# Performance work log

Measured on AMD Instinct MI355X. Metric: run time of the kernel, lower is better.

The kernel has to match this reference:

```python
import jax, jax.numpy as jnp
import numpy as np

S, N, D, K, NH = 4, 32768, 256, 512, 4
HD = D // NH  # head dim 64
F = 4 * D     # ffn hidden
EPS = 1e-6


def layer_norm(x, g, b):
    mu = x.mean(-1, keepdims=True)
    var = x.var(-1, keepdims=True)
    return (x - mu) * jax.lax.rsqrt(var + 1e-5) * g + b


def setup_inputs() -> dict:
    key = jax.random.key(0)
    ks = jax.random.split(key, 16)
    w = lambda i, shape: jax.random.normal(ks[i], shape, jnp.float32) * 0.02
    return {
        "H_nodes": jax.random.normal(ks[0], (S, N, D), jnp.float32),
        "patch_ids": jax.random.randint(ks[1], (S, N), 0, K),
        "ln1_g": jnp.ones((D,), jnp.float32), "ln1_b": jnp.zeros((D,), jnp.float32),
        "Wq": w(2, (D, D)), "bq": jnp.zeros((D,), jnp.float32),
        "Wk": w(3, (D, D)), "bk": jnp.zeros((D,), jnp.float32),
        "Wv": w(4, (D, D)), "bv": jnp.zeros((D,), jnp.float32),
        "Wo": w(5, (D, D)), "bo": jnp.zeros((D,), jnp.float32),
        "ln2_g": jnp.ones((D,), jnp.float32), "ln2_b": jnp.zeros((D,), jnp.float32),
        "ffn_W1": w(6, (D, F)), "ffn_b1": jnp.zeros((F,), jnp.float32),
        "ffn_W2": w(7, (F, D)), "ffn_b2": jnp.zeros((D,), jnp.float32),
        "mlp_W1": w(8, (2 * D, D)), "mlp_b1": jnp.zeros((D,), jnp.float32),
        "mlp_W2": w(9, (D, D)), "mlp_b2": jnp.zeros((D,), jnp.float32),
    }


def reference(H_nodes, patch_ids, ln1_g, ln1_b, Wq, bq, Wk, bk, Wv, bv, Wo, bo,
              ln2_g, ln2_b, ffn_W1, ffn_b1, ffn_W2, ffn_b2,
              mlp_W1, mlp_b1, mlp_W2, mlp_b2):
    # --- segment-mean pooling by patch id (replaces double python loop) ---
    flat_ids = (patch_ids + jnp.arange(S)[:, None] * K).reshape(-1)  # [S*N]
    sums = jax.ops.segment_sum(H_nodes.reshape(S * N, D), flat_ids,
                               num_segments=S * K).reshape(S, K, D)
    counts = jax.ops.segment_sum(jnp.ones((S * N,), H_nodes.dtype), flat_ids,
                                 num_segments=S * K).reshape(S, K, 1)
    x = sums / jnp.maximum(counts, 1.0)         # empty patches stay zero
    mask = (counts > 0).astype(H_nodes.dtype)   # [S,K,1]

    # --- linear-attention transformer block over patch summaries (eval: no dropout) ---
    y = layer_norm(x, ln1_g, ln1_b)
    phi = lambda t: jax.nn.elu(t) + 1.0
    q = phi((y @ Wq + bq).reshape(S, K, NH, HD))
    k = phi((y @ Wk + bk).reshape(S, K, NH, HD)) * mask[..., None]
    v = (y @ Wv + bv).reshape(S, K, NH, HD) * mask[..., None]
    kv = jnp.einsum('skhd,skhe->shde', k, v)
    ksum = k.sum(axis=1)                                    # [S,NH,HD]
    num = jnp.einsum('skhd,shde->skhe', q, kv)
    den = jnp.einsum('skhd,shd->skh', q, ksum)[..., None] + EPS
    x = x + (num / den).reshape(S, K, D) @ Wo + bo
    y2 = layer_norm(x, ln2_g, ln2_b)
    psu = x + jax.nn.gelu(y2 @ ffn_W1 + ffn_b1, approximate=False) @ ffn_W2 + ffn_b2

    # --- gather-broadcast + concat + node MLP + residual ---
    bc = jax.vmap(lambda p, i: p[i])(psu, patch_ids)        # [S,N,D]
    combined = jnp.concatenate([H_nodes, bc], axis=-1)      # [S,N,2D]
    upd = jax.nn.gelu(combined @ mlp_W1 + mlp_b1, approximate=False) @ mlp_W2 + mlp_b2
    return H_nodes + upd, psu
```

## Files before the change

### kernel.cpp

```cpp
#include <hip/hip_runtime.h>
#include <hip/hip_bf16.h>

#define S 4
#define N 32768
#define D 256
#define KSEG 512
#define NH 4
#define HD 64
#define FF 1024

typedef __attribute__((ext_vector_type(8))) short short8;
typedef __attribute__((ext_vector_type(4))) float f32x4;
typedef __attribute__((ext_vector_type(4))) unsigned int u32x4;
typedef __attribute__((ext_vector_type(2))) unsigned int u32x2;

__device__ __forceinline__ unsigned short f2bf(float f) {
  union { __hip_bfloat16 h; unsigned short u; } cv;
  cv.h = __float2bfloat16(f);
  return cv.u;
}

__device__ __forceinline__ float gelu_f(float x) {
  return 0.5f * x * (1.0f + erff(x * 0.70710678118654752440f));
}

__device__ __forceinline__ float wave_reduce_sum(float v) {
  #pragma unroll
  for (int o = 32; o > 0; o >>= 1) v += __shfl_xor(v, o, 64);
  return v;
}

__global__ __launch_bounds__(256) void hist_kernel(
    const int* __restrict__ pids, int* __restrict__ histc)
{
  __shared__ int h[KSEG];
  int b = blockIdx.x, t = threadIdx.x;
  int s = b >> 4, c = b & 15;
  for (int i = t; i < KSEG; i += 256) h[i] = 0;
  __syncthreads();
  const int* p = pids + s * N + c * 2048;
  for (int i = t; i < 2048; i += 256) atomicAdd(&h[p[i]], 1);
  __syncthreads();
  for (int i = t; i < KSEG; i += 256) histc[(s * 16 + c) * KSEG + i] = h[i];
}

__global__ __launch_bounds__(256) void prefix_kernel(
    int* __restrict__ histc, int* __restrict__ segstart,
    int* __restrict__ cnti, float* __restrict__ counts)
{
  __shared__ int h[16 * KSEG];
  __shared__ int sc[KSEG];
  __shared__ int sa[KSEG], sb[KSEG];
  int s = blockIdx.x, t = threadIdx.x;
  for (int i = t; i < 16 * KSEG; i += 256) h[i] = histc[s * 16 * KSEG + i];
  __syncthreads();
  #pragma unroll
  for (int u = 0; u < 2; u++) {
    int bin = t + u * 256;
    int cc = 0;
    #pragma unroll
    for (int c = 0; c < 16; c++) cc += h[c * KSEG + bin];
    sc[bin] = cc;
    sa[bin] = cc;
  }
  __syncthreads();
  int* src = sa; int* dst = sb;
  for (int off = 1; off < KSEG; off <<= 1) {
    #pragma unroll
    for (int u = 0; u < 2; u++) {
      int bin = t + u * 256;
      int v = src[bin];
      if (bin >= off) v += src[bin - off];
      dst[bin] = v;
    }
    __syncthreads();
    int* tmp = src; src = dst; dst = tmp;
  }
  #pragma unroll
  for (int u = 0; u < 2; u++) {
    int bin = t + u * 256;
    int cc = sc[bin];
    int excl = src[bin] - cc;
    segstart[s * KSEG + bin] = excl;
    cnti[s * KSEG + bin] = cc;
    counts[s * KSEG + bin] = (float)cc;
    int run = excl;
    #pragma unroll
    for (int c = 0; c < 16; c++) {
      int v = h[c * KSEG + bin];
      h[c * KSEG + bin] = run;
      run += v;
    }
  }
  __syncthreads();
  for (int i = t; i < 16 * KSEG; i += 256) histc[s * 16 * KSEG + i] = h[i];
}

__global__ __launch_bounds__(256) void scatter_kernel(
    const int* __restrict__ pids, const int* __restrict__ histc,
    int* __restrict__ order)
{
  __shared__ int offs[KSEG];
  int b = blockIdx.x, t = threadIdx.x;
  int s = b >> 4, c = b & 15;
  for (int i = t; i < KSEG; i += 256) offs[i] = histc[(s * 16 + c) * KSEG + i];
  __syncthreads();
  const int* p = pids + s * N + c * 2048;
  for (int i = t; i < 2048; i += 256) {
    int pid = p[i];
    int pos = atomicAdd(&offs[pid], 1);
    order[s * N + pos] = s * N + c * 2048 + i;
  }
}

__global__ __launch_bounds__(256) void pool_gather(
    const float* __restrict__ H, const int* __restrict__ order,
    const int* __restrict__ segstart, const int* __restrict__ cnti,
    float* __restrict__ xw)
{
  __shared__ float pbuf[4][256];
  int tid = threadIdx.x;
  int w = tid >> 6, lane = tid & 63;
  int seg = blockIdx.x * 2 + (w >> 1);
  int half = w & 1;
  int s = seg >> 9;
  int st = segstart[seg], cn = cnti[seg];
  int en = st + cn;
  const int* ord = order + (size_t)s * N;
  int c4 = lane << 2;
  f32x4 a0 = {0,0,0,0}, a1 = {0,0,0,0}, a2 = {0,0,0,0}, a3 = {0,0,0,0};
  f32x4 a4 = {0,0,0,0}, a5 = {0,0,0,0}, a6 = {0,0,0,0}, a7 = {0,0,0,0};
  int i = st + half;
  for (; i + 14 < en; i += 16) {
    int r0 = ord[i + 0], r1 = ord[i + 2], r2 = ord[i + 4], r3 = ord[i + 6];
    int r4 = ord[i + 8], r5 = ord[i + 10], r6 = ord[i + 12], r7 = ord[i + 14];
    a0 += *(const f32x4*)(H + (size_t)r0 * 256 + c4);
    a1 += *(const f32x4*)(H + (size_t)r1 * 256 + c4);
    a2 += *(const f32x4*)(H + (size_t)r2 * 256 + c4);
    a3 += *(const f32x4*)(H + (size_t)r3 * 256 + c4);
    a4 += *(const f32x4*)(H + (size_t)r4 * 256 + c4);
    a5 += *(const f32x4*)(H + (size_t)r5 * 256 + c4);
    a6 += *(const f32x4*)(H + (size_t)r6 * 256 + c4);
    a7 += *(const f32x4*)(H + (size_t)r7 * 256 + c4);
  }
  for (; i < en; i += 2) {
    int r = ord[i];
    a0 += *(const f32x4*)(H + (size_t)r * 256 + c4);
  }
  f32x4 ssum = ((a0 + a1) + (a2 + a3)) + ((a4 + a5) + (a6 + a7));
  *(f32x4*)&pbuf[w][c4] = ssum;
  __syncthreads();
  if (half == 0) {
    f32x4 tot = *(f32x4*)&pbuf[w][c4];
    tot += *(f32x4*)&pbuf[w + 1][c4];
    float inv = 1.f / fmaxf((float)cn, 1.f);
    tot = tot * inv;
    *(f32x4*)(xw + (size_t)seg * 256 + c4) = tot;
  }
}

__global__ __launch_bounds__(256) void pool_ln_kernel(
    const float* __restrict__ xw,
    const float* __restrict__ g, const float* __restrict__ b,
    float* __restrict__ yw)
{
  int row = blockIdx.x, t = threadIdx.x;
  float v = xw[row * 256 + t];
  float s1 = wave_reduce_sum(v);
  float s2 = wave_reduce_sum(v * v);
  __shared__ float a1[4], a2[4];
  int w = t >> 6;
  if ((t & 63) == 0) { a1[w] = s1; a2[w] = s2; }
  __syncthreads();
  float ts1 = a1[0] + a1[1] + a1[2] + a1[3];
  float ts2 = a2[0] + a2[1] + a2[2] + a2[3];
  float mu = ts1 * (1.f / 256.f);
  float var = ts2 * (1.f / 256.f) - mu * mu;
  yw[row * 256 + t] = (v - mu) * rsqrtf(var + 1e-5f) * g[t] + b[t];
}

__global__ __launch_bounds__(256) void ln_kernel(
    const float* __restrict__ in, float* __restrict__ outp,
    const float* __restrict__ g, const float* __restrict__ b)
{
  int row = blockIdx.x, t = threadIdx.x;
  float v = in[row * 256 + t];
  float s1 = wave_reduce_sum(v);
  float s2 = wave_reduce_sum(v * v);
  __shared__ float a1[4], a2[4];
  int w = t >> 6;
  if ((t & 63) == 0) { a1[w] = s1; a2[w] = s2; }
  __syncthreads();
  float ts1 = a1[0] + a1[1] + a1[2] + a1[3];
  float ts2 = a2[0] + a2[1] + a2[2] + a2[3];
  float mu = ts1 * (1.f / 256.f);
  float var = ts2 * (1.f / 256.f) - mu * mu;
  outp[row * 256 + t] = (v - mu) * rsqrtf(var + 1e-5f) * g[t] + b[t];
}

__global__ __launch_bounds__(256) void wprep2_kernel(
    const float* __restrict__ Wq, const float* __restrict__ Wk,
    const float* __restrict__ Wv, const float* __restrict__ Wo,
    const float* __restrict__ fW1, const float* __restrict__ fW2,
    const float* __restrict__ mW1, const float* __restrict__ mW2,
    unsigned short* __restrict__ Wpack)
{
  int fi = blockIdx.x * 256 + threadIdx.x;
  const float* src; int ld, colbase, kcbits; size_t outb; int rfi;
  if (fi < 32768) {
    int m = fi >> 13; rfi = fi & 8191;
    src = (m == 0) ? Wq : ((m == 1) ? Wk : ((m == 2) ? Wv : Wo));
    ld = 256; colbase = 0; kcbits = 3; outb = (size_t)m * 65536;
  } else if (fi < 65536) {
    rfi = fi - 32768; int cc = rfi >> 13; rfi &= 8191;
    src = fW1; ld = 1024; colbase = cc * 256; kcbits = 3;
    outb = 262144 + (size_t)cc * 65536;
  } else if (fi < 98304) {
    rfi = fi - 65536; src = fW2; ld = 256; colbase = 0; kcbits = 5; outb = 524288;
  } else if (fi < 114688) {
    rfi = fi - 98304; src = mW1; ld = 256; colbase = 0; kcbits = 4; outb = 786432;
  } else {
    rfi = fi - 114688; src = mW2; ld = 256; colbase = 0; kcbits = 3; outb = 917504;
  }
  int tile = rfi >> 6, lane = rfi & 63;
  int c = tile >> kcbits, kc = tile & ((1 << kcbits) - 1);
  int k0 = kc * 32 + (lane >> 4) * 8;
  int col = colbase + c * 16 + (lane & 15);
  unsigned int p[4];
  #pragma unroll
  for (int jj = 0; jj < 4; jj++) {
    unsigned int lo = f2bf(src[(size_t)(k0 + 2 * jj) * ld + col]);
    unsigned int hi = f2bf(src[(size_t)(k0 + 2 * jj + 1) * ld + col]);
    p[jj] = lo | (hi << 16);
  }
  u32x4 v = {p[0], p[1], p[2], p[3]};
  *(u32x4*)&Wpack[outb + (size_t)rfi * 8] = v;
}

#define AP3 264
#define CP3 260

__global__ __launch_bounds__(256, 4) void qkv_mfma(
    const float* __restrict__ y, const float* __restrict__ counts,
    const unsigned short* __restrict__ Wpack,
    const float* __restrict__ bq, const float* __restrict__ bk,
    const float* __restrict__ bv,
    float* __restrict__ qo, float* __restrict__ ko, float* __restrict__ vo)
{
  __shared__ __align__(16) unsigned char smem[16 * CP3 * 4];
  unsigned short* Ah = (unsigned short*)smem;
  float* Cl = (float*)smem;
  int m = blockIdx.y;
  const unsigned short* Wf = Wpack + (size_t)m * 65536;
  const float* bias = (m == 0) ? bq : ((m == 1) ? bk : bv);
  float* outp = (m == 0) ? qo : ((m == 1) ? ko : vo);
  int tid = threadIdx.x, lane = tid & 63, w = tid >> 6;
  int ln15 = lane & 15, hi = lane >> 4;
  int base = blockIdx.x * 16;

  for (int i = tid; i < 16 * 64; i += 256) {
    int r = i >> 6, c4 = i & 63;
    float4 f = *(const float4*)(y + ((size_t)(base + r)) * 256 + c4 * 4);
    unsigned int lo = (unsigned int)f2bf(f.x) | ((unsigned int)f2bf(f.y) << 16);
    unsigned int h2 = (unsigned int)f2bf(f.z) | ((unsigned int)f2bf(f.w) << 16);
    u32x2 val = {lo, h2};
    *((u32x2*)&Ah[r * AP3 + c4 * 4]) = val;
  }
  __syncthreads();

  f32x4 acc[4];
  #pragma unroll
  for (int c = 0; c < 4; c++) acc[c] = (f32x4){0.f, 0.f, 0.f, 0.f};
  const unsigned short* Wl = Wf + (size_t)lane * 8;
  short8 bcur[4];
  #pragma unroll
  for (int ct = 0; ct < 4; ct++)
    bcur[ct] = *(const short8*)(Wl + ((w * 4 + ct) * 8 + 0) * 512);
  #pragma unroll
  for (int kc = 0; kc < 8; kc++) {
    short8 a = *(const short8*)(&Ah[ln15 * AP3 + kc * 32 + hi * 8]);
    short8 bnext[4];
    if (kc < 7) {
      #pragma unroll
      for (int ct = 0; ct < 4; ct++)
        bnext[ct] = *(const short8*)(Wl + ((w * 4 + ct) * 8 + kc + 1) * 512);
    }
    #pragma unroll
    for (int ct = 0; ct < 4; ct++)
      acc[ct] = __builtin_amdgcn_mfma_f32_16x16x32_bf16(a, bcur[ct], acc[ct], 0, 0, 0);
    if (kc < 7) {
      #pragma unroll
      for (int ct = 0; ct < 4; ct++) bcur[ct] = bnext[ct];
    }
  }
  __syncthreads();

  float mk[4];
  #pragma unroll
  for (int r = 0; r < 4; r++)
    mk[r] = (counts[base + hi * 4 + r] > 0.f) ? 1.f : 0.f;
  #pragma unroll
  for (int ct = 0; ct < 4; ct++) {
    int col = w * 64 + ct * 16 + ln15;
    float bb = bias[col];
    #pragma unroll
    for (int r = 0; r < 4; r++) {
      float tv = acc[ct][r] + bb;
      if (m <= 1) tv = (tv > 0.f) ? (tv + 1.f) : expf(tv);
      if (m >= 1) tv *= mk[r];
      Cl[(hi * 4 + r) * CP3 + col] = tv;
    }
  }
  __syncthreads();
  for (int i = tid; i < 16 * 64; i += 256) {
    int r = i >> 6, c4 = i & 63;
    *(float4*)(outp + ((size_t)(base + r)) * 256 + c4 * 4) =
        *(const float4*)&Cl[r * CP3 + c4 * 4];
  }
}

__global__ __launch_bounds__(256, 4) void oproj_mfma(
    const float* __restrict__ aw, const float* __restrict__ xw,
    const unsigned short* __restrict__ Wpack, const float* __restrict__ bo,
    float* __restrict__ x2)
{
  __shared__ __align__(16) unsigned char smem[16 * CP3 * 4];
  unsigned short* Ah = (unsigned short*)smem;
  float* Cl = (float*)smem;
  const unsigned short* Wf = Wpack + 196608;
  int tid = threadIdx.x, lane = tid & 63, w = tid >> 6;
  int ln15 = lane & 15, hi = lane >> 4;
  int base = blockIdx.x * 16;

  for (int i = tid; i < 16 * 64; i += 256) {
    int r = i >> 6, c4 = i & 63;
    float4 f = *(const float4*)(aw + ((size_t)(base + r)) * 256 + c4 * 4);
    unsigned int lo = (unsigned int)f2bf(f.x) | ((unsigned int)f2bf(f.y) << 16);
    unsigned int h2 = (unsigned int)f2bf(f.z) | ((unsigned int)f2bf(f.w) << 16);
    u32x2 val = {lo, h2};
    *((u32x2*)&Ah[r * AP3 + c4 * 4]) = val;
  }
  __syncthreads();

  f32x4 acc[4];
  #pragma unroll
  for (int c = 0; c < 4; c++) acc[c] = (f32x4){0.f, 0.f, 0.f, 0.f};
  const unsigned short* Wl = Wf + (size_t)lane * 8;
  short8 bcur[4];
  #pragma unroll
  for (int ct = 0; ct < 4; ct++)
    bcur[ct] = *(const short8*)(Wl + ((w * 4 + ct) * 8 + 0) * 512);
  #pragma unroll
  for (int kc = 0; kc < 8; kc++) {
    short8 a = *(const short8*)(&Ah[ln15 * AP3 + kc * 32 + hi * 8]);
    short8 bnext[4];
    if (kc < 7) {
      #pragma unroll
      for (int ct = 0; ct < 4; ct++)
        bnext[ct] = *(const short8*)(Wl + ((w * 4 + ct) * 8 + kc + 1) * 512);
    }
    #pragma unroll
    for (int ct = 0; ct < 4; ct++)
      acc[ct] = __builtin_amdgcn_mfma_f32_16x16x32_bf16(a, bcur[ct], acc[ct], 0, 0, 0);
    if (kc < 7) {
      #pragma unroll
      for (int ct = 0; ct < 4; ct++) bcur[ct] = bnext[ct];
    }
  }
  __syncthreads();

  #pragma unroll
  for (int ct = 0; ct < 4; ct++) {
    int col = w * 64 + ct * 16 + ln15;
    float bb = bo[col];
    #pragma unroll
    for (int r = 0; r < 4; r++)
      Cl[(hi * 4 + r) * CP3 + col] = acc[ct][r] + bb;
  }
  __syncthreads();
  for (int i = tid; i < 16 * 64; i += 256) {
    int r = i >> 6, c4 = i & 63;
    size_t gidx = ((size_t)(base + r)) * 256 + c4 * 4;
    float4 xv = *(const float4*)(xw + gidx);
    float4 cv = *(const float4*)&Cl[r * CP3 + c4 * 4];
    float4 o = {xv.x + cv.x, xv.y + cv.y, xv.z + cv.z, xv.w + cv.w};
    *(float4*)(x2 + gidx) = o;
  }
}

__global__ __launch_bounds__(256, 4) void ffn1_mfma(
    const float* __restrict__ y2, const unsigned short* __restrict__ Wpack,
    const float* __restrict__ b1, unsigned short* __restrict__ hidb)
{
  __shared__ __align__(16) unsigned char smem[16 * CP3 * 4];
  unsigned short* Ah = (unsigned short*)smem;
  int cc = blockIdx.y;
  const unsigned short* Wf = Wpack + 262144 + (size_t)cc * 65536;
  int tid = threadIdx.x, lane = tid & 63, w = tid >> 6;
  int ln15 = lane & 15, hi = lane >> 4;
  int base = blockIdx.x * 16;

  for (int i = tid; i < 16 * 64; i += 256) {
    int r = i >> 6, c4 = i & 63;
    float4 f = *(const float4*)(y2 + ((size_t)(base + r)) * 256 + c4 * 4);
    unsigned int lo = (unsigned int)f2bf(f.x) | ((unsigned int)f2bf(f.y) << 16);
    unsigned int h2 = (unsigned int)f2bf(f.z) | ((unsigned int)f2bf(f.w) << 16);
    u32x2 val = {lo, h2};
    *((u32x2*)&Ah[r * AP3 + c4 * 4]) = val;
  }
  __syncthreads();

  f32x4 acc[4];
  #pragma unroll
  for (int c = 0; c < 4; c++) acc[c] = (f32x4){0.f, 0.f, 0.f, 0.f};
  const unsigned short* Wl = Wf + (size_t)lane * 8;
  short8 bcur[4];
  #pragma unroll
  for (int ct = 0; ct < 4; ct++)
    bcur[ct] = *(const short8*)(Wl + ((w * 4 + ct) * 8 + 0) * 512);
  #pragma unroll
  for (int kc = 0; kc < 8; kc++) {
    short8 a = *(const short8*)(&Ah[ln15 * AP3 + kc * 32 + hi * 8]);
    short8 bnext[4];
    if (kc < 7) {
      #pragma unroll
      for (int ct = 0; ct < 4; ct++)
        bnext[ct] = *(const short8*)(Wl + ((w * 4 + ct) * 8 + kc + 1) * 512);
    }
    #pragma unroll
    for (int ct = 0; ct < 4; ct++)
      acc[ct] = __builtin_amdgcn_mfma_f32_16x16x32_bf16(a, bcur[ct], acc[ct], 0, 0, 0);
    if (kc < 7) {
      #pragma unroll
      for (int ct = 0; ct < 4; ct++) bcur[ct] = bnext[ct];
    }
  }
  __syncthreads();

  #pragma unroll
  for (int ct = 0; ct < 4; ct++) {
    int col = w * 64 + ct * 16 + ln15;
    float bb = b1[cc * 256 + col];
    #pragma unroll
    for (int r = 0; r < 4; r++)
      Ah[(hi * 4 + r) * 256 + col] = f2bf(gelu_f(acc[ct][r] + bb));
  }
  __syncthreads();
  for (int i = tid; i < 16 * 32; i += 256) {
    int r = i >> 5, c8 = i & 31;
    *(u32x4*)(hidb + ((size_t)(base + r)) * FF + cc * 256 + c8 * 8) =
        *(const u32x4*)&Ah[r * 256 + c8 * 8];
  }
}

__global__ __launch_bounds__(256, 4) void ffn2_mfma(
    const unsigned short* __restrict__ hidb, const float* __restrict__ x2,
    const unsigned short* __restrict__ Wpack, const float* __restrict__ b2,
    float* __restrict__ psu_out, unsigned short* __restrict__ psub)
{
  __shared__ __align__(16) unsigned char smem[16 * CP3 * 4];
  unsigned short* Ah = (unsigned short*)smem;
  float* Cl = (float*)smem;
  const unsigned short* Wf = Wpack + 524288;
  int tid = threadIdx.x, lane = tid & 63, w = tid >> 6;
  int ln15 = lane & 15, hi = lane >> 4;
  int base = blockIdx.x * 16;

  f32x4 acc[4];
  #pragma unroll
  for (int c = 0; c < 4; c++) acc[c] = (f32x4){0.f, 0.f, 0.f, 0.f};
  const unsigned short* Wl = Wf + (size_t)lane * 8;

  for (int ch = 0; ch < 4; ch++) {
    __syncthreads();
    for (int i = tid; i < 16 * 32; i += 256) {
      int r = i >> 5, c8 = i & 31;
      *((u32x4*)&Ah[r * AP3 + c8 * 8]) =
          *(const u32x4*)(hidb + ((size_t)(base + r)) * FF + ch * 256 + c8 * 8);
    }
    __syncthreads();
    short8 bcur[4];
    #pragma unroll
    for (int ct = 0; ct < 4; ct++)
      bcur[ct] = *(const short8*)(Wl + ((w * 4 + ct) * 32 + ch * 8 + 0) * 512);
    #pragma unroll
    for (int kc = 0; kc < 8; kc++) {
      short8 a = *(const short8*)(&Ah[ln15 * AP3 + kc * 32 + hi * 8]);
      short8 bnext[4];
      if (kc < 7) {
        #pragma unroll
        for (int ct = 0; ct < 4; ct++)
          bnext[ct] = *(const short8*)(Wl + ((w * 4 + ct) * 32 + ch * 8 + kc + 1) * 512);
      }
      #pragma unroll
      for (int ct = 0; ct < 4; ct++)
        acc[ct] = __builtin_amdgcn_mfma_f32_16x16x32_bf16(a, bcur[ct], acc[ct], 0, 0, 0);
      if (kc < 7) {
        #pragma unroll
        for (int ct = 0; ct < 4; ct++) bcur[ct] = bnext[ct];
      }
    }
  }
  __syncthreads();

  #pragma unroll
  for (int ct = 0; ct < 4; ct++) {
    int col = w * 64 + ct * 16 + ln15;
    float bb = b2[col];
    #pragma unroll
    for (int r = 0; r < 4; r++)
      Cl[(hi * 4 + r) * CP3 + col] = acc[ct][r] + bb;
  }
  __syncthreads();
  for (int i = tid; i < 16 * 64; i += 256) {
    int r = i >> 6, c4 = i & 63;
    size_t gidx = ((size_t)(base + r)) * 256 + c4 * 4;
    float4 xv = *(const float4*)(x2 + gidx);
    float4 cv = *(const float4*)&Cl[r * CP3 + c4 * 4];
    float4 o = {xv.x + cv.x, xv.y + cv.y, xv.z + cv.z, xv.w + cv.w};
    *(float4*)(psu_out + gidx) = o;
    unsigned int lo = (unsigned int)f2bf(o.x) | ((unsigned int)f2bf(o.y) << 16);
    unsigned int h2 = (unsigned int)f2bf(o.z) | ((unsigned int)f2bf(o.w) << 16);
    u32x2 pb = {lo, h2};
    *(u32x2*)(psub + gidx) = pb;
  }
}

__global__ __launch_bounds__(256) void kv_kernel(
    const float* __restrict__ kw, const float* __restrict__ vw,
    float* __restrict__ kvb, float* __restrict__ ksb)
{
  int b = blockIdx.x, t = threadIdx.x;
  int s = b / (NH * 8), h = (b / 8) % NH, ck = b & 7;
  __shared__ float kl[64 * 64];
  __shared__ float vl[64 * 64];
  for (int i = t; i < 4096; i += 256) {
    int kk = i >> 6, d = i & 63;
    size_t rowb = ((size_t)(s * KSEG + ck * 64 + kk) * NH + h) * HD + d;
    kl[i] = kw[rowb];
    vl[i] = vw[rowb];
  }
  __syncthreads();
  int d = t & 63, eb = (t >> 6) * 16;
  f32x4 a4[4];
  #pragma unroll
  for (int j = 0; j < 4; j++) a4[j] = (f32x4){0.f, 0.f, 0.f, 0.f};
  float acck = 0.f;
  #pragma unroll 4
  for (int kk = 0; kk < 64; kk++) {
    float kd = kl[kk * 64 + d];
    acck += kd;
    #pragma unroll
    for (int j = 0; j < 4; j++) {
      f32x4 vv = *(const f32x4*)&vl[kk * 64 + eb + j * 4];
      a4[j] += kd * vv;
    }
  }
  #pragma unroll
  for (int j = 0; j < 4; j++)
    #pragma unroll
    for (int e = 0; e < 4; e++)
      atomicAdd(&kvb[(((size_t)(s * NH + h)) * HD + d) * HD + eb + j * 4 + e], a4[j][e]);
  if (t < 64) atomicAdd(&ksb[(s * NH + h) * HD + t], acck);
}

__global__ __launch_bounds__(256) void attn_kernel(
    const float* __restrict__ qw, const float* __restrict__ kvb,
    const float* __restrict__ ksb, float* __restrict__ aw)
{
  __shared__ float kvl[64 * 64];
  __shared__ float ksl[64];
  __shared__ float ql[32 * 64];
  int t = threadIdx.x, b = blockIdx.x;
  int sh = b >> 4, rb = b & 15;
  int s = sh >> 2, h = sh & 3;
  for (int i = t; i < 4096; i += 256) kvl[i] = kvb[sh * 4096 + i];
  if (t < 64) ksl[t] = ksb[sh * 64 + t];
  for (int i = t; i < 2048; i += 256) {
    int r = i >> 6, d = i & 63;
    ql[i] = qw[((size_t)(s * KSEG + rb * 32 + r)) * 256 + h * 64 + d];
  }
  __syncthreads();
  int e = t & 63, rg = t >> 6;
  float num[8], den[8];
  #pragma unroll
  for (int r = 0; r < 8; r++) { num[r] = 0.f; den[r] = 0.f; }
  #pragma unroll 4
  for (int d4 = 0; d4 < 64; d4 += 4) {
    float4 ks4 = *(const float4*)&ksl[d4];
    float kv0 = kvl[(d4 + 0) * 64 + e];
    float kv1 = kvl[(d4 + 1) * 64 + e];
    float kv2 = kvl[(d4 + 2) * 64 + e];
    float kv3 = kvl[(d4 + 3) * 64 + e];
    #pragma unroll
    for (int r = 0; r < 8; r++) {
      float4 q4 = *(const float4*)&ql[(rg * 8 + r) * 64 + d4];
      num[r] += q4.x * kv0 + q4.y * kv1 + q4.z * kv2 + q4.w * kv3;
      den[r] += q4.x * ks4.x + q4.y * ks4.y + q4.z * ks4.z + q4.w * ks4.w;
    }
  }
  #pragma unroll
  for (int r = 0; r < 8; r++) {
    int row = rb * 32 + rg * 8 + r;
    aw[((size_t)(s * KSEG + row)) * 256 + h * 64 + e] = num[r] / (den[r] + 1e-6f);
  }
}

#define AP2 264
#define CP2 260
__global__ __launch_bounds__(256, 5) void node_mlp_kernel(
    const float* __restrict__ H, const int* __restrict__ pids,
    const unsigned short* __restrict__ psub,
    const unsigned short* __restrict__ W1f, const unsigned short* __restrict__ W2f,
    const float* __restrict__ b1, const float* __restrict__ b2,
    float* __restrict__ out)
{
  __shared__ __align__(16) unsigned char smem[32 * AP2 * 2];
  __shared__ int pidl[32];
  unsigned short* Ah = (unsigned short*)smem;
  float* Cl = (float*)smem;
  int tid = threadIdx.x;
  int lane = tid & 63, w = tid >> 6;
  int ln15 = lane & 15, hi = lane >> 4;
  int base = blockIdx.x * 32;

  f32x4 acc[2][4];
  #pragma unroll
  for (int a = 0; a < 2; a++)
    #pragma unroll
    for (int c = 0; c < 4; c++) acc[a][c] = (f32x4){0.f, 0.f, 0.f, 0.f};

  if (tid < 32) pidl[tid] = pids[base + tid];
  for (int i = tid; i < 32 * 64; i += 256) {
    int r = i >> 6, c4 = i & 63;
    float4 f = *(const float4*)(H + ((size_t)(base + r)) * 256 + c4 * 4);
    unsigned int lo = (unsigned int)f2bf(f.x) | ((unsigned int)f2bf(f.y) << 16);
    unsigned int hi2 = (unsigned int)f2bf(f.z) | ((unsigned int)f2bf(f.w) << 16);
    u32x2 val = {lo, hi2};
    *((u32x2*)&Ah[r * AP2 + c4 * 4]) = val;
  }
  __syncthreads();

  const unsigned short* Wl1 = W1f + (size_t)lane * 8;
  {
    short8 bcur[4];
    #pragma unroll
    for (int ct = 0; ct < 4; ct++)
      bcur[ct] = *(const short8*)(Wl1 + ((w * 4 + ct) * 16 + 0) * 512);
    #pragma unroll
    for (int kc = 0; kc < 8; kc++) {
      short8 a[2], bnext[4];
      #pragma unroll
      for (int rt = 0; rt < 2; rt++)
        a[rt] = *(const short8*)(&Ah[(rt * 16 + ln15) * AP2 + kc * 32 + hi * 8]);
      #pragma unroll
      for (int ct = 0; ct < 4; ct++)
        bnext[ct] = *(const short8*)(Wl1 + ((w * 4 + ct) * 16 + kc + 1) * 512);
      __builtin_amdgcn_s_setprio(1);
      #pragma unroll
      for (int rt = 0; rt < 2; rt++)
        #pragma unroll
        for (int ct = 0; ct < 4; ct++)
          acc[rt][ct] = __builtin_amdgcn_mfma_f32_16x16x32_bf16(a[rt], bcur[ct], acc[rt][ct], 0, 0, 0);
      __builtin_amdgcn_s_setprio(0);
      #pragma unroll
      for (int ct = 0; ct < 4; ct++) bcur[ct] = bnext[ct];
    }
  }
  __syncthreads();

  for (int i = tid; i < 32 * 32; i += 256) {
    int r = i >> 5, ch = i & 31;
    int node = base + r;
    int ss = node >> 15;
    int pid = pidl[r];
    *((u32x4*)&Ah[r * AP2 + ch * 8]) =
        *(const u32x4*)(psub + ((size_t)(ss * KSEG + pid)) * 256 + ch * 8);
  }
  __syncthreads();

  {
    short8 bcur[4];
    #pragma unroll
    for (int ct = 0; ct < 4; ct++)
      bcur[ct] = *(const short8*)(Wl1 + ((w * 4 + ct) * 16 + 8) * 512);
    #pragma unroll
    for (int kc = 8; kc < 16; kc++) {
      short8 a[2], bnext[4];
      #pragma unroll
      for (int rt = 0; rt < 2; rt++)
        a[rt] = *(const short8*)(&Ah[(rt * 16 + ln15) * AP2 + (kc - 8) * 32 + hi * 8]);
      if (kc < 15) {
        #pragma unroll
        for (int ct = 0; ct < 4; ct++)
          bnext[ct] = *(const short8*)(Wl1 + ((w * 4 + ct) * 16 + kc + 1) * 512);
      }
      __builtin_amdgcn_s_setprio(1);
      #pragma unroll
      for (int rt = 0; rt < 2; rt++)
        #pragma unroll
        for (int ct = 0; ct < 4; ct++)
          acc[rt][ct] = __builtin_amdgcn_mfma_f32_16x16x32_bf16(a[rt], bcur[ct], acc[rt][ct], 0, 0, 0);
      __builtin_amdgcn_s_setprio(0);
      if (kc < 15) {
        #pragma unroll
        for (int ct = 0; ct < 4; ct++) bcur[ct] = bnext[ct];
      }
    }
  }
  __syncthreads();

  #pragma unroll
  for (int rt = 0; rt < 2; rt++) {
    #pragma unroll
    for (int ct = 0; ct < 4; ct++) {
      int col = w * 64 + ct * 16 + ln15;
      float bb = b1[col];
      #pragma unroll
      for (int r = 0; r < 4; r++) {
        int row = rt * 16 + hi * 4 + r;
        Ah[row * AP2 + col] = f2bf(gelu_f(acc[rt][ct][r] + bb));
      }
      acc[rt][ct] = (f32x4){0.f, 0.f, 0.f, 0.f};
    }
  }
  __syncthreads();

  {
    const unsigned short* Wl2 = W2f + (size_t)lane * 8;
    short8 bcur[4];
    #pragma unroll
    for (int ct = 0; ct < 4; ct++)
      bcur[ct] = *(const short8*)(Wl2 + ((w * 4 + ct) * 8 + 0) * 512);
    #pragma unroll
    for (int kc = 0; kc < 8; kc++) {
      short8 a[2], bnext[4];
      #pragma unroll
      for (int rt = 0; rt < 2; rt++)
        a[rt] = *(const short8*)(&Ah[(rt * 16 + ln15) * AP2 + kc * 32 + hi * 8]);
      if (kc < 7) {
        #pragma unroll
        for (int ct = 0; ct < 4; ct++)
          bnext[ct] = *(const short8*)(Wl2 + ((w * 4 + ct) * 8 + kc + 1) * 512);
      }
      __builtin_amdgcn_s_setprio(1);
      #pragma unroll
      for (int rt = 0; rt < 2; rt++)
        #pragma unroll
        for (int ct = 0; ct < 4; ct++)
          acc[rt][ct] = __builtin_amdgcn_mfma_f32_16x16x32_bf16(a[rt], bcur[ct], acc[rt][ct], 0, 0, 0);
      __builtin_amdgcn_s_setprio(0);
      if (kc < 7) {
        #pragma unroll
        for (int ct = 0; ct < 4; ct++) bcur[ct] = bnext[ct];
      }
    }
  }

  #pragma unroll
  for (int rh = 0; rh < 2; rh++) {
    __syncthreads();
    #pragma unroll
    for (int ct = 0; ct < 4; ct++) {
      int col = w * 64 + ct * 16 + ln15;
      float bb = b2[col];
      #pragma unroll
      for (int r = 0; r < 4; r++)
        Cl[(hi * 4 + r) * CP2 + col] = acc[rh][ct][r] + bb;
    }
    __syncthreads();
    for (int i = tid; i < 16 * 64; i += 256) {
      int r = i >> 6, c4 = i & 63;
      size_t gidx = ((size_t)(base + rh * 16 + r)) * 256 + c4 * 4;
      float4 h4 = *(const float4*)(H + gidx);
      float4 cv = *(const float4*)&Cl[r * CP2 + c4 * 4];
      float4 o4 = {h4.x + cv.x, h4.y + cv.y, h4.z + cv.z, h4.w + cv.w};
      *(float4*)(out + gidx) = o4;
    }
  }
}

extern "C" void kernel_launch(void* const* d_in, const int* in_sizes, int n_in,
                              void* d_out, int out_size, void* d_ws, size_t ws_size,
                              hipStream_t stream) {
  (void)in_sizes; (void)n_in; (void)out_size; (void)ws_size;
  const float* H    = (const float*)d_in[0];
  const int*   pids = (const int*)d_in[1];
  const float* ln1g = (const float*)d_in[2];
  const float* ln1b = (const float*)d_in[3];
  const float* Wq   = (const float*)d_in[4];
  const float* bq   = (const float*)d_in[5];
  const float* Wk   = (const float*)d_in[6];
  const float* bk   = (const float*)d_in[7];
  const float* Wv   = (const float*)d_in[8];
  const float* bv   = (const float*)d_in[9];
  const float* Wo   = (const float*)d_in[10];
  const float* bo   = (const float*)d_in[11];
  const float* ln2g = (const float*)d_in[12];
  const float* ln2b = (const float*)d_in[13];
  const float* fW1  = (const float*)d_in[14];
  const float* fb1  = (const float*)d_in[15];
  const float* fW2  = (const float*)d_in[16];
  const float* fb2  = (const float*)d_in[17];
  const float* mW1  = (const float*)d_in[18];
  const float* mb1  = (const float*)d_in[19];
  const float* mW2  = (const float*)d_in[20];
  const float* mb2  = (const float*)d_in[21];
  float* out = (float*)d_out;
  float* ws = (float*)d_ws;

  int*   histc   = (int*)ws;
  int*   segstart= (int*)(ws + 32768);
  int*   cnti    = (int*)(ws + 34816);
  int*   order   = (int*)(ws + 36864);
  float* counts  = ws + 167936;
  float* xw      = ws + 169984;
  float* yw      = ws + 694272;
  float* qw      = ws + 1218560;
  float* kw      = ws + 1742848;
  float* vw      = ws + 2267136;
  float* kvb     = ws + 2791424;
  float* ksb     = ws + 2856960;
  float* aw      = ws + 2857984;
  float* x2w     = ws + 3382272;
  float* y2w     = ws + 3906560;
  unsigned short* hidb  = (unsigned short*)(ws + 4430848);
  unsigned short* psub  = (unsigned short*)(ws + 5479424);
  unsigned short* Wpack = (unsigned short*)(ws + 5741568);

  hipMemsetAsync(kvb, 0, (65536 + 1024) * sizeof(float), stream);

  wprep2_kernel<<<480, 256, 0, stream>>>(Wq, Wk, Wv, Wo, fW1, fW2, mW1, mW2, Wpack);
  hist_kernel<<<64, 256, 0, stream>>>(pids, histc);
  prefix_kernel<<<4, 256, 0, stream>>>(histc, segstart, cnti, counts);
  scatter_kernel<<<64, 256, 0, stream>>>(pids, histc, order);
  pool_gather<<<1024, 256, 0, stream>>>(H, order, segstart, cnti, xw);
  pool_ln_kernel<<<2048, 256, 0, stream>>>(xw, ln1g, ln1b, yw);
  qkv_mfma<<<dim3(128, 3), 256, 0, stream>>>(yw, counts, Wpack, bq, bk, bv, qw, kw, vw);
  kv_kernel<<<128, 256, 0, stream>>>(kw, vw, kvb, ksb);
  attn_kernel<<<256, 256, 0, stream>>>(qw, kvb, ksb, aw);
  oproj_mfma<<<128, 256, 0, stream>>>(aw, xw, Wpack, bo, x2w);
  ln_kernel<<<2048, 256, 0, stream>>>(x2w, y2w, ln2g, ln2b);
  ffn1_mfma<<<dim3(128, 4), 256, 0, stream>>>(y2w, Wpack, fb1, hidb);
  ffn2_mfma<<<128, 256, 0, stream>>>(hidb, x2w, Wpack, fb2,
                                     out + (size_t)S * N * D, psub);
  node_mlp_kernel<<<4096, 256, 0, stream>>>(H, pids, psub,
                                            Wpack + 786432, Wpack + 917504,
                                            mb1, mb2, out);
}
```

Baseline: 237.8 us.

## Fuse layer norms into pooling and o-proj, streamline node MLP epilogue

Result: slower. 772.8 us (+225.0%).

```diff
diff --git a/kernel.cpp b/kernel.cpp
--- a/kernel.cpp
+++ b/kernel.cpp
@@ -116,7 +116,8 @@
 __global__ __launch_bounds__(256) void pool_gather(
     const float* __restrict__ H, const int* __restrict__ order,
     const int* __restrict__ segstart, const int* __restrict__ cnti,
-    float* __restrict__ xw)
+    const float* __restrict__ g, const float* __restrict__ bta,
+    float* __restrict__ xw, float* __restrict__ yw)
 {
   __shared__ float pbuf[4][256];
   int tid = threadIdx.x;
@@ -156,46 +157,19 @@
     float inv = 1.f / fmaxf((float)cn, 1.f);
     tot = tot * inv;
     *(f32x4*)(xw + (size_t)seg * 256 + c4) = tot;
-  }
-}
-
-__global__ __launch_bounds__(256) void pool_ln_kernel(
-    const float* __restrict__ xw,
-    const float* __restrict__ g, const float* __restrict__ b,
-    float* __restrict__ yw)
-{
-  int row = blockIdx.x, t = threadIdx.x;
-  float v = xw[row * 256 + t];
-  float s1 = wave_reduce_sum(v);
-  float s2 = wave_reduce_sum(v * v);
-  __shared__ float a1[4], a2[4];
-  int w = t >> 6;
-  if ((t & 63) == 0) { a1[w] = s1; a2[w] = s2; }
-  __syncthreads();
-  float ts1 = a1[0] + a1[1] + a1[2] + a1[3];
-  float ts2 = a2[0] + a2[1] + a2[2] + a2[3];
-  float mu = ts1 * (1.f / 256.f);
-  float var = ts2 * (1.f / 256.f) - mu * mu;
-  yw[row * 256 + t] = (v - mu) * rsqrtf(var + 1e-5f) * g[t] + b[t];
-}
-
-__global__ __launch_bounds__(256) void ln_kernel(
-    const float* __restrict__ in, float* __restrict__ outp,
-    const float* __restrict__ g, const float* __restrict__ b)
-{
-  int row = blockIdx.x, t = threadIdx.x;
-  float v = in[row * 256 + t];
-  float s1 = wave_reduce_sum(v);
-  float s2 = wave_reduce_sum(v * v);
-  __shared__ float a1[4], a2[4];
-  int w = t >> 6;
-  if ((t & 63) == 0) { a1[w] = s1; a2[w] = s2; }
-  __syncthreads();
-  float ts1 = a1[0] + a1[1] + a1[2] + a1[3];
-  float ts2 = a2[0] + a2[1] + a2[2] + a2[3];
-  float mu = ts1 * (1.f / 256.f);
-  float var = ts2 * (1.f / 256.f) - mu * mu;
-  outp[row * 256 + t] = (v - mu) * rsqrtf(var + 1e-5f) * g[t] + b[t];
+    float s1 = tot[0] + tot[1] + tot[2] + tot[3];
+    float s2 = tot[0]*tot[0] + tot[1]*tot[1] + tot[2]*tot[2] + tot[3]*tot[3];
+    s1 = wave_reduce_sum(s1);
+    s2 = wave_reduce_sum(s2);
+    float mu = s1 * (1.f / 256.f);
+    float var = s2 * (1.f / 256.f) - mu * mu;
+    float rs = rsqrtf(var + 1e-5f);
+    float4 g4 = *(const float4*)(g + c4);
+    float4 b4 = *(const float4*)(bta + c4);
+    float4 yv = {(tot[0]-mu)*rs*g4.x + b4.x, (tot[1]-mu)*rs*g4.y + b4.y,
+                 (tot[2]-mu)*rs*g4.z + b4.z, (tot[3]-mu)*rs*g4.w + b4.w};
+    *(float4*)(yw + (size_t)seg * 256 + c4) = yv;
+  }
 }
 
 __global__ __launch_bounds__(256) void wprep2_kernel(
@@ -322,7 +296,8 @@
 __global__ __launch_bounds__(256, 4) void oproj_mfma(
     const float* __restrict__ aw, const float* __restrict__ xw,
     const unsigned short* __restrict__ Wpack, const float* __restrict__ bo,
-    float* __restrict__ x2)
+    const float* __restrict__ g, const float* __restrict__ bta,
+    float* __restrict__ x2, float* __restrict__ y2)
 {
   __shared__ __align__(16) unsigned char smem[16 * CP3 * 4];
   unsigned short* Ah = (unsigned short*)smem;
@@ -378,13 +353,27 @@
       Cl[(hi * 4 + r) * CP3 + col] = acc[ct][r] + bb;
   }
   __syncthreads();
-  for (int i = tid; i < 16 * 64; i += 256) {
-    int r = i >> 6, c4 = i & 63;
-    size_t gidx = ((size_t)(base + r)) * 256 + c4 * 4;
-    float4 xv = *(const float4*)(xw + gidx);
-    float4 cv = *(const float4*)&Cl[r * CP3 + c4 * 4];
-    float4 o = {xv.x + cv.x, xv.y + cv.y, xv.z + cv.z, xv.w + cv.w};
-    *(float4*)(x2 + gidx) = o;
+  int c4 = lane << 2;
+  float4 g4 = *(const float4*)(g + c4);
+  float4 b4 = *(const float4*)(bta + c4);
+  #pragma unroll
+  for (int k = 0; k < 4; k++) {
+    int r = k * 4 + w;
+    size_t gbase = ((size_t)(base + r)) * 256 + c4;
+    float4 xv = *(const float4*)(xw + gbase);
+    float4 cv = *(const float4*)&Cl[r * CP3 + c4];
+    float4 x2v = {xv.x + cv.x, xv.y + cv.y, xv.z + cv.z, xv.w + cv.w};
+    *(float4*)(x2 + gbase) = x2v;
+    float s1 = x2v.x + x2v.y + x2v.z + x2v.w;
+    float s2 = x2v.x*x2v.x + x2v.y*x2v.y + x2v.z*x2v.z + x2v.w*x2v.w;
+    s1 = wave_reduce_sum(s1);
+    s2 = wave_reduce_sum(s2);
+    float mu = s1 * (1.f / 256.f);
+    float var = s2 * (1.f / 256.f) - mu * mu;
+    float rs = rsqrtf(var + 1e-5f);
+    float4 yv = {(x2v.x-mu)*rs*g4.x + b4.x, (x2v.y-mu)*rs*g4.y + b4.y,
+                 (x2v.z-mu)*rs*g4.z + b4.z, (x2v.w-mu)*rs*g4.w + b4.w};
+    *(float4*)(y2 + gbase) = yv;
   }
 }
 
@@ -607,18 +596,15 @@
 }
 
 #define AP2 264
-#define CP2 260
-__global__ __launch_bounds__(256, 5) void node_mlp_kernel(
+__global__ __launch_bounds__(256, 7) void node_mlp_kernel(
     const float* __restrict__ H, const int* __restrict__ pids,
     const unsigned short* __restrict__ psub,
     const unsigned short* __restrict__ W1f, const unsigned short* __restrict__ W2f,
     const float* __restrict__ b1, const float* __restrict__ b2,
     float* __restrict__ out)
 {
-  __shared__ __align__(16) unsigned char smem[32 * AP2 * 2];
+  __shared__ __align__(16) unsigned short Ah[32 * AP2];
   __shared__ int pidl[32];
-  unsigned short* Ah = (unsigned short*)smem;
-  float* Cl = (float*)smem;
   int tid = threadIdx.x;
   int lane = tid & 63, w = tid >> 6;
   int ln15 = lane & 15, hi = lane >> 4;
@@ -631,7 +617,9 @@
     for (int c = 0; c < 4; c++) acc[a][c] = (f32x4){0.f, 0.f, 0.f, 0.f};
 
   if (tid < 32) pidl[tid] = pids[base + tid];
-  for (int i = tid; i < 32 * 64; i += 256) {
+  #pragma unroll
+  for (int k = 0; k < 8; k++) {
+    int i = tid + k * 256;
     int r = i >> 6, c4 = i & 63;
     float4 f = *(const float4*)(H + ((size_t)(base + r)) * 256 + c4 * 4);
     unsigned int lo = (unsigned int)f2bf(f.x) | ((unsigned int)f2bf(f.y) << 16);
@@ -653,9 +641,11 @@
       #pragma unroll
       for (int rt = 0; rt < 2; rt++)
         a[rt] = *(const short8*)(&Ah[(rt * 16 + ln15) * AP2 + kc * 32 + hi * 8]);
-      #pragma unroll
-      for (int ct = 0; ct < 4; ct++)
-        bnext[ct] = *(const short8*)(Wl1 + ((w * 4 + ct) * 16 + kc + 1) * 512);
+      if (kc < 7) {
+        #pragma unroll
+        for (int ct = 0; ct < 4; ct++)
+          bnext[ct] = *(const short8*)(Wl1 + ((w * 4 + ct) * 16 + kc + 1) * 512);
+      }
       __builtin_amdgcn_s_setprio(1);
       #pragma unroll
       for (int rt = 0; rt < 2; rt++)
@@ -663,20 +653,26 @@
         for (int ct = 0; ct < 4; ct++)
           acc[rt][ct] = __builtin_amdgcn_mfma_f32_16x16x32_bf16(a[rt], bcur[ct], acc[rt][ct], 0, 0, 0);
       __builtin_amdgcn_s_setprio(0);
-      #pragma unroll
-      for (int ct = 0; ct < 4; ct++) bcur[ct] = bnext[ct];
-    }
-  }
-  __syncthreads();
-
-  for (int i = tid; i < 32 * 32; i += 256) {
-    int r = i >> 5, ch = i & 31;
-    int node = base + r;
-    int ss = node >> 15;
-    int pid = pidl[r];
-    *((u32x4*)&Ah[r * AP2 + ch * 8]) =
-        *(const u32x4*)(psub + ((size_t)(ss * KSEG + pid)) * 256 + ch * 8);
-  }
+      if (kc < 7) {
+        #pragma unroll
+        for (int ct = 0; ct < 4; ct++) bcur[ct] = bnext[ct];
+      }
+    }
+  }
+
+  int ss = base >> 15;
+  int r0 = tid >> 5, ch = tid & 31;
+  int p0 = pidl[r0], p1 = pidl[8 + r0], p2 = pidl[16 + r0], p3 = pidl[24 + r0];
+  const unsigned short* pbase = psub + (size_t)(ss * KSEG) * 256 + (size_t)ch * 8;
+  u32x4 g0 = *(const u32x4*)(pbase + (size_t)p0 * 256);
+  u32x4 g1 = *(const u32x4*)(pbase + (size_t)p1 * 256);
+  u32x4 g2 = *(const u32x4*)(pbase + (size_t)p2 * 256);
+  u32x4 g3 = *(const u32x4*)(pbase + (size_t)p3 * 256);
+  __syncthreads();
+  *(u32x4*)&Ah[r0 * AP2 + ch * 8] = g0;
+  *(u32x4*)&Ah[(8 + r0) * AP2 + ch * 8] = g1;
+  *(u32x4*)&Ah[(16 + r0) * AP2 + ch * 8] = g2;
+  *(u32x4*)&Ah[(24 + r0) * AP2 + ch * 8] = g3;
   __syncthreads();
 
   {
@@ -758,24 +754,24 @@
   }
 
   #pragma unroll
-  for (int rh = 0; rh < 2; rh++) {
-    __syncthreads();
+  for (int rt = 0; rt < 2; rt++) {
+    float hv[16];
+    #pragma unroll
+    for (int ct = 0; ct < 4; ct++) {
+      int col = w * 64 + ct * 16 + ln15;
+      #pragma unroll
+      for (int r = 0; r < 4; r++)
+        hv[ct * 4 + r] = H[((size_t)(base + rt * 16 + hi * 4 + r)) * 256 + col];
+    }
     #pragma unroll
     for (int ct = 0; ct < 4; ct++) {
       int col = w * 64 + ct * 16 + ln15;
       float bb = b2[col];
       #pragma unroll
-      for (int r = 0; r < 4; r++)
-        Cl[(hi * 4 + r) * CP2 + col] = acc[rh][ct][r] + bb;
-    }
-    __syncthreads();
-    for (int i = tid; i < 16 * 64; i += 256) {
-      int r = i >> 6, c4 = i & 63;
-      size_t gidx = ((size_t)(base + rh * 16 + r)) * 256 + c4 * 4;
-      float4 h4 = *(const float4*)(H + gidx);
-      float4 cv = *(const float4*)&Cl[r * CP2 + c4 * 4];
-      float4 o4 = {h4.x + cv.x, h4.y + cv.y, h4.z + cv.z, h4.w + cv.w};
-      *(float4*)(out + gidx) = o4;
+      for (int r = 0; r < 4; r++) {
+        size_t gi = ((size_t)(base + rt * 16 + hi * 4 + r)) * 256 + col;
+        out[gi] = hv[ct * 4 + r] + acc[rt][ct][r] + bb;
+      }
     }
   }
 }
@@ -834,13 +830,11 @@
   hist_kernel<<<64, 256, 0, stream>>>(pids, histc);
   prefix_kernel<<<4, 256, 0, stream>>>(histc, segstart, cnti, counts);
   scatter_kernel<<<64, 256, 0, stream>>>(pids, histc, order);
-  pool_gather<<<1024, 256, 0, stream>>>(H, order, segstart, cnti, xw);
-  pool_ln_kernel<<<2048, 256, 0, stream>>>(xw, ln1g, ln1b, yw);
+  pool_gather<<<1024, 256, 0, stream>>>(H, order, segstart, cnti, ln1g, ln1b, xw, yw);
   qkv_mfma<<<dim3(128, 3), 256, 0, stream>>>(yw, counts, Wpack, bq, bk, bv, qw, kw, vw);
   kv_kernel<<<128, 256, 0, stream>>>(kw, vw, kvb, ksb);
   attn_kernel<<<256, 256, 0, stream>>>(qw, kvb, ksb, aw);
-  oproj_mfma<<<128, 256, 0, stream>>>(aw, xw, Wpack, bo, x2w);
-  ln_kernel<<<2048, 256, 0, stream>>>(x2w, y2w, ln2g, ln2b);
+  oproj_mfma<<<128, 256, 0, stream>>>(aw, xw, Wpack, bo, ln2g, ln2b, x2w, y2w);
   ffn1_mfma<<<dim3(128, 4), 256, 0, stream>>>(y2w, Wpack, fb1, hidb);
   ffn2_mfma<<<128, 256, 0, stream>>>(hidb, x2w, Wpack, fb2,
                                      out + (size_t)S * N * D, psub);
```
